# Kernel tuning notes

Hardware: AMD Instinct MI355X
Metric: run time of the kernel (lower is better)

Reference implementation:

```python
import jax, jax.numpy as jnp
import numpy as np

K_POOL = 5

def _conv_lookahead(x, W):
    # Faithful to F.conv2d(pad=(fs//2+1,0)) followed by keeping the last L rows:
    # for fs=3 this reduces to out[t] = sum_j x[t+j] @ W[:,j,:].T (2 trailing zeros).
    # x: [..., L, E], W: [nf, fs, E] -> out [..., L, nf]
    fs = W.shape[1]
    L = x.shape[-2]
    pad = [(0, 0)] * (x.ndim - 2) + [(0, fs - 1), (0, 0)]
    xp = jnp.pad(x, pad)
    out = sum(jnp.einsum('...le,fe->...lf', jax.lax.dynamic_slice_in_dim(xp, j, L, axis=-2), W[:, j, :]) for j in range(fs))
    return out

def _cosine(q, s):
    # q: [B,Q,D], s: [B,S,L,D] -> [B,S,Q,L]
    num = jnp.einsum('bqd,bsld->bsql', q, s)
    qn = jnp.linalg.norm(q, axis=-1)  # [B,Q]
    sn = jnp.linalg.norm(s, axis=-1)  # [B,S,L]
    return num / (qn[:, None, :, None] * sn[:, :, None, :])

def _pool(sim, k=K_POOL):
    # sort-based k-max pooling over last dim -> (max, mean-of-top-k), matching torch.sort + slice
    top = jax.lax.top_k(sim, k)[0]            # [..., Q, k] descending
    return jnp.stack([top[..., 0], top.mean(-1)], axis=-1)  # [..., Q, 2]

def _bce(p, t):
    return -(t * jnp.log(p) + (1.0 - t) * jnp.log(1.0 - p)).mean()

def setup_inputs() -> dict:
    key = jax.random.key(0)
    ks = jax.random.split(key, 9)
    B, S, L, Q, V, E, NF, FS = 16, 48, 64, 32, 50000, 300, 256, 3
    return {
        'sentences': jax.random.randint(ks[0], (B, S, L), 0, V, dtype=jnp.int64 if jax.config.jax_enable_x64 else jnp.int32).astype(jnp.int32),
        'question': jax.random.randint(ks[1], (B, Q), 0, V).astype(jnp.int32),
        'target_sents': jax.random.randint(ks[2], (B, S), 0, 2).astype(jnp.int32),
        'target_docs': jax.random.randint(ks[3], (B,), 0, 2).astype(jnp.int32),
        'similarity_one_hot': jax.random.uniform(ks[4], (B, S, Q, L), dtype=jnp.float32),
        'embeds': jax.random.normal(ks[5], (V, E), dtype=jnp.float32),
        'conv_w': jax.random.normal(ks[6], (NF, FS, E), dtype=jnp.float32),
        'lin_w': jax.random.normal(ks[7], (1, 6), dtype=jnp.float32),
        'lin_b': jax.random.normal(ks[8], (1,), dtype=jnp.float32),
    }

def reference(sentences, question, target_sents, target_docs, similarity_one_hot, embeds, conv_w, lin_w, lin_b):
    q_emb = embeds[question]            # [B,Q,E]
    s_emb = embeds[sentences]           # [B,S,L,E]
    q_conv = _conv_lookahead(q_emb, conv_w)   # [B,Q,NF]
    s_conv = _conv_lookahead(s_emb, conv_w)   # [B,S,L,NF]

    sim_ins = _cosine(q_emb, s_emb)     # [B,S,Q,L]
    qmask = (question > 1).astype(sim_ins.dtype)   # [B,Q]
    smask = (sentences > 1).astype(sim_ins.dtype)  # [B,S,L]
    sim_ins = sim_ins * qmask[:, None, :, None] * smask[:, :, None, :]

    sim_sens = _cosine(q_conv, s_conv)  # [B,S,Q,L]

    feats = jnp.concatenate([_pool(sim_ins), _pool(sim_sens), _pool(similarity_one_hot)], axis=-1)  # [B,S,Q,6]
    lo = jax.nn.sigmoid(jnp.einsum('bsqf,of->bsqo', feats, lin_w)[..., 0] + lin_b[0])  # [B,S,Q]
    sent_output = lo.mean(-1)           # [B,S]

    sal = _bce(sent_output, target_sents.astype(sent_output.dtype))
    doc_emit = sent_output.max(-1)      # [B]
    dal = _bce(doc_emit, target_docs.astype(doc_emit.dtype))
    total_loss = (sal + dal) / 2.0
    return (total_loss, sent_output, doc_emit)
```

## Files before the change

### kernel.cpp

```cpp
#include <hip/hip_runtime.h>
#include <math.h>

#define NB 16
#define NS 48
#define NL 64
#define NQ 32
#define NE 300
#define NF 256
#define KP 320
#define QROWS 36

typedef __attribute__((ext_vector_type(8))) short short8;
typedef __attribute__((ext_vector_type(4))) float f32x4;

#define MFMA(a,b,c) __builtin_amdgcn_mfma_f32_16x16x32_bf16((a),(b),(c),0,0,0)

__device__ __forceinline__ unsigned short f2bf(float f) {
    unsigned u = __float_as_uint(f);
    u += 0x7fff + ((u >> 16) & 1);
    return (unsigned short)(u >> 16);
}

#define SE_PITCH 640
#define SC_PITCH 512
#define SIM_OFF (66 * 640)
#define SIM_PITCH 66
#define DYN_LDS (SIM_OFF + NQ * SIM_PITCH * 4)

__device__ __forceinline__ float wave_reduce_sum(float v) {
#pragma unroll
    for (int off = 32; off; off >>= 1) v += __shfl_xor(v, off, 64);
    return v;
}

__device__ __forceinline__ void top5_pool4(float v0, float v1, float v2, float v3,
                                           int lane, float* mx, float* mn) {
    float s0 = 0.f, s1 = 0.f, s2 = 0.f, s3 = 0.f;
    float x0 = 0.f, x1 = 0.f, x2 = 0.f, x3 = 0.f;
#pragma unroll
    for (int i = 0; i < 5; ++i) {
        float m0 = v0, m1 = v1, m2 = v2, m3 = v3;
#pragma unroll
        for (int off = 32; off; off >>= 1) {
            m0 = fmaxf(m0, __shfl_xor(m0, off, 64));
            m1 = fmaxf(m1, __shfl_xor(m1, off, 64));
            m2 = fmaxf(m2, __shfl_xor(m2, off, 64));
            m3 = fmaxf(m3, __shfl_xor(m3, off, 64));
        }
        if (i == 0) { x0 = m0; x1 = m1; x2 = m2; x3 = m3; }
        s0 += m0; s1 += m1; s2 += m2; s3 += m3;
        unsigned long long k0 = __ballot(v0 == m0);
        unsigned long long k1 = __ballot(v1 == m1);
        unsigned long long k2 = __ballot(v2 == m2);
        unsigned long long k3 = __ballot(v3 == m3);
        if (lane == __ffsll(k0) - 1) v0 = -3.4e38f;
        if (lane == __ffsll(k1) - 1) v1 = -3.4e38f;
        if (lane == __ffsll(k2) - 1) v2 = -3.4e38f;
        if (lane == __ffsll(k3) - 1) v3 = -3.4e38f;
    }
    mx[0] = x0; mx[1] = x1; mx[2] = x2; mx[3] = x3;
    mn[0] = s0 * 0.2f; mn[1] = s1 * 0.2f; mn[2] = s2 * 0.2f; mn[3] = s3 * 0.2f;
}

__global__ __launch_bounds__(256) void prep_kernel(
        const float* __restrict__ conv_w, const int* __restrict__ question,
        const float* __restrict__ embeds,
        short8* __restrict__ Wb2, unsigned short* __restrict__ qe,
        short8* __restrict__ qef, float* __restrict__ q_norm,
        float* __restrict__ qcssq, unsigned int* __restrict__ done_ctr) {
    int blk = blockIdx.x;
    int tid = threadIdx.x;
    if (blk < 120) {
        if (blk == 0 && tid == 0) done_ctr[0] = 0u;
        int i = blk * 256 + tid;
        if (i < NB * NQ) qcssq[i] = 0.f;
        int rl = i & 15;
        int ftile = (i >> 4) & 15;
        int c = i >> 8;
        int kg = c & 3, rest = c >> 2;
        int ks = rest % 10, j = rest / 10;
        int f = ftile * 16 + rl;
        int k0 = ks * 32 + kg * 8;
        const float* src = conv_w + (size_t)(f * 3 + j) * NE;
        short8 h;
#pragma unroll
        for (int e = 0; e < 8; ++e) {
            int k = k0 + e;
            h[e] = (short)((k < NE) ? f2bf(src[k]) : (unsigned short)0);
        }
        Wb2[i] = h;
    } else {
        int row = (blk - 120) * 4 + (tid >> 6);
        int b = row / QROWS, r = row % QROWS;
        int l = tid & 63;
        unsigned short* dst = qe + (size_t)row * KP;
        if (r < NQ) {
            int tok = question[b * NQ + r];
            const float4* rp = (const float4*)(embeds + (size_t)tok * NE);
            short8 h = {0, 0, 0, 0, 0, 0, 0, 0};
            float ss = 0.f;
            if (l < 38) {
                float4 v0 = rp[2 * l];
                ss += v0.x * v0.x + v0.y * v0.y + v0.z * v0.z + v0.w * v0.w;
                h[0] = (short)f2bf(v0.x); h[1] = (short)f2bf(v0.y);
                h[2] = (short)f2bf(v0.z); h[3] = (short)f2bf(v0.w);
                if (2 * l + 1 < 75) {
                    float4 v1 = rp[2 * l + 1];
                    ss += v1.x * v1.x + v1.y * v1.y + v1.z * v1.z + v1.w * v1.w;
                    h[4] = (short)f2bf(v1.x); h[5] = (short)f2bf(v1.y);
                    h[6] = (short)f2bf(v1.z); h[7] = (short)f2bf(v1.w);
                }
            }
            if (l < 40) {
                *(short8*)(dst + 8 * l) = h;
                qef[((size_t)(b * 2 + (r >> 4)) * 40 + l) * 16 + (r & 15)] = h;
            }
            ss = wave_reduce_sum(ss);
            if (l == 0) q_norm[b * NQ + r] = sqrtf(ss);
        } else {
            if (l < 40) {
                short8 z = {0, 0, 0, 0, 0, 0, 0, 0};
                *(short8*)(dst + 8 * l) = z;
            }
        }
    }
}

__global__ __launch_bounds__(256) void qconv_mfma_kernel(
        const unsigned short* __restrict__ qe, const short8* __restrict__ Wb2,
        short8* __restrict__ qcf, float* __restrict__ qcssq) {
    __shared__ unsigned short tile[NQ][72];
    int b = blockIdx.x >> 2, fq = blockIdx.x & 3;
    int tid = threadIdx.x, lane = tid & 63, w = tid >> 6;
    int rl = lane & 15, kg = lane >> 4;
    int ftile = fq * 4 + w;
    f32x4 acc0 = (f32x4){0.f, 0.f, 0.f, 0.f};
    f32x4 acc1 = (f32x4){0.f, 0.f, 0.f, 0.f};
    for (int j = 0; j < 3; ++j) {
#pragma unroll 2
        for (int ks = 0; ks < 10; ++ks) {
            int k = ks * 32 + kg * 8;
            int c = (j * 10 + ks) * 4 + kg;
            short8 a0 = *(const short8*)(qe + ((size_t)(b * QROWS) + rl + j) * KP + k);
            short8 a1 = *(const short8*)(qe + ((size_t)(b * QROWS) + 16 + rl + j) * KP + k);
            short8 bb = Wb2[(c * 16 + ftile) * 16 + rl];
            acc0 = MFMA(a0, bb, acc0);
            acc1 = MFMA(a1, bb, acc1);
        }
    }
    int fl = w * 16 + rl;
#pragma unroll
    for (int reg = 0; reg < 4; ++reg) {
        tile[kg * 4 + reg][fl] = f2bf(acc0[reg]);
        tile[16 + kg * 4 + reg][fl] = f2bf(acc1[reg]);
    }
    __syncthreads();
    {
        int mh = tid >> 7, c_local = (tid >> 4) & 7, rl2 = tid & 15;
        short8 h = *(const short8*)(&tile[mh * 16 + rl2][c_local * 8]);
        qcf[((size_t)(b * 2 + mh) * 32 + 8 * fq + c_local) * 16 + rl2] = h;
    }
    {
        int qq = tid >> 3, fgrp = tid & 7;
        short8 h = *(const short8*)(&tile[qq][fgrp * 8]);
        float ss = 0.f;
#pragma unroll
        for (int e = 0; e < 8; ++e) {
            float v = __uint_as_float(((unsigned)(unsigned short)h[e]) << 16);
            ss += v * v;
        }
        ss += __shfl_xor(ss, 1, 64);
        ss += __shfl_xor(ss, 2, 64);
        ss += __shfl_xor(ss, 4, 64);
        if (fgrp == 0) atomicAdd(&qcssq[b * NQ + qq], ss);
    }
}

extern __shared__ char ldsc[];
__global__ __launch_bounds__(256, 3) void fused8_kernel(
    const int* __restrict__ sentences, const int* __restrict__ question,
    const float* __restrict__ sim_oh, const float* __restrict__ embeds,
    const short8* __restrict__ Wb2,
    const short8* __restrict__ qef, const short8* __restrict__ qcf,
    const float* __restrict__ q_norm, const float* __restrict__ qcssq,
    const float* __restrict__ lin_w, const float* __restrict__ lin_b,
    const int* __restrict__ tsent, const int* __restrict__ tdoc,
    unsigned int* __restrict__ done_ctr,
    float* __restrict__ sent_ws, float* __restrict__ d_out)
{
    __shared__ int toks[NL];
    __shared__ float smaskf[NL], snorm[NL], scnorm[NL];
    __shared__ float qn_s[NQ], qcn_s[NQ], qmf_s[NQ];
    __shared__ float wq[4];
    __shared__ float fpool[NQ][2];
    __shared__ int lastflag;
    __shared__ float red2[4];
    __shared__ float dred[NB];

    int tid = threadIdx.x, lane = tid & 63, w = tid >> 6;
    int rl = lane & 15, kg = lane >> 4;
    int bs = blockIdx.x, b = bs / NS;
    int t = (w << 4) + rl, t7 = t & 7;

    float oh[8];
#pragma unroll
    for (int qi = 0; qi < 8; ++qi) {
        int q = (w << 3) + qi;
        oh[qi] = sim_oh[((size_t)bs * NQ + q) * NL + lane];
    }

    if (tid < NL) {
        int tk = sentences[(size_t)bs * NL + tid];
        toks[tid] = tk;
        smaskf[tid] = (tk > 1) ? 1.f : 0.f;
    } else if (tid < NL + NQ) {
        int q = tid - NL;
        qn_s[q] = q_norm[b * NQ + q];
    } else if (tid < NL + 2 * NQ) {
        int q = tid - NL - NQ;
        qcn_s[q] = sqrtf(qcssq[b * NQ + q]);
    } else if (tid < NL + 3 * NQ) {
        int q = tid - NL - 2 * NQ;
        qmf_s[q] = (question[b * NQ + q] > 1) ? 1.f : 0.f;
    }
    __syncthreads();

#pragma unroll 4
    for (int i = 0; i < 16; ++i) {
        int r = (i << 2) + w;
        char* rowbase = ldsc + r * SE_PITCH;
        int m7 = r & 7;
        const float4* rp = (const float4*)(embeds + (size_t)toks[r] * NE);
        {
            float4 v = rp[lane];
            ushort4 h = {f2bf(v.x), f2bf(v.y), f2bf(v.z), f2bf(v.w)};
            *(ushort4*)(rowbase + (((lane >> 1) ^ m7) << 4) + ((lane & 1) << 3)) = h;
        }
        if (lane < 11) {
            float4 v = rp[64 + lane];
            ushort4 h = {f2bf(v.x), f2bf(v.y), f2bf(v.z), f2bf(v.w)};
            int g = 64 + lane;
            *(ushort4*)(rowbase + (((g >> 1) ^ m7) << 4) + ((g & 1) << 3)) = h;
        }
        if (lane < 5) {
            int pk = 37 + ((lane + 1) >> 1);
            int sub = ((lane + 1) & 1) << 3;
            *(unsigned long long*)(rowbase + ((pk ^ m7) << 4) + sub) = 0ull;
        }
    }
    if (w < 2) {
        int r = 64 + w;
        if (lane < 40) {
            uint4 z = {0, 0, 0, 0};
            *(uint4*)(ldsc + r * SE_PITCH + (lane << 4)) = z;
        }
    }
    __syncthreads();

    {
        f32x4 iacc0 = (f32x4){0.f, 0.f, 0.f, 0.f};
        f32x4 iacc1 = (f32x4){0.f, 0.f, 0.f, 0.f};
        f32x4 nB = (f32x4){0.f, 0.f, 0.f, 0.f};
        const short8* qf = qef + (size_t)(b * 80) * 16;
#pragma unroll 2
        for (int ks = 0; ks < 10; ++ks) {
            int c = ks * 4 + kg;
            short8 bB = *(const short8*)(ldsc + t * SE_PITCH + ((c ^ t7) << 4));
            short8 a0 = qf[c * 16 + rl];
            short8 a1 = qf[(40 + c) * 16 + rl];
            iacc0 = MFMA(a0, bB, iacc0);
            iacc1 = MFMA(a1, bB, iacc1);
            nB = MFMA(bB, bB, nB);
        }
        if (kg == (rl >> 2)) snorm[t] = sqrtf(nB[rl & 3]);
        __syncthreads();

        float inv_t = smaskf[t] / snorm[t];
#pragma unroll
        for (int reg = 0; reg < 4; ++reg) {
            int q0 = kg * 4 + reg;
            float s0 = iacc0[reg] / qn_s[q0] * inv_t * qmf_s[q0];
            *(float*)(ldsc + SIM_OFF + (q0 * SIM_PITCH + t) * 4) = s0;
            int q1 = 16 + kg * 4 + reg;
            float s1 = iacc1[reg] / qn_s[q1] * inv_t * qmf_s[q1];
            *(float*)(ldsc + SIM_OFF + (q1 * SIM_PITCH + t) * 4) = s1;
        }
    }
    __syncthreads();

    {
        int q0 = w << 3;
        float v[8];
#pragma unroll
        for (int qi = 0; qi < 8; ++qi)
            v[qi] = *(float*)(ldsc + SIM_OFF + ((q0 + qi) * SIM_PITCH + lane) * 4);
        float mx[4], mn[4];
        top5_pool4(v[0], v[1], v[2], v[3], lane, mx, mn);
        if (lane == 0)
#pragma unroll
            for (int p = 0; p < 4; ++p) { fpool[q0 + p][0] = mx[p]; fpool[q0 + p][1] = mn[p]; }
        top5_pool4(v[4], v[5], v[6], v[7], lane, mx, mn);
        if (lane == 0)
#pragma unroll
            for (int p = 0; p < 4; ++p) { fpool[q0 + 4 + p][0] = mx[p]; fpool[q0 + 4 + p][1] = mn[p]; }
    }

    f32x4 cacc[4][4];
#pragma unroll
    for (int m = 0; m < 4; ++m)
#pragma unroll
        for (int nn = 0; nn < 4; ++nn) cacc[m][nn] = (f32x4){0.f, 0.f, 0.f, 0.f};
    for (int j = 0; j < 3; ++j) {
#pragma unroll 2
        for (int ks = 0; ks < 10; ++ks) {
            int c = (j * 10 + ks) * 4 + kg;
            short8 a[4], bb[4];
#pragma unroll
            for (int m = 0; m < 4; ++m) {
                int row = m * 16 + rl + j;
                a[m] = *(const short8*)(ldsc + row * SE_PITCH +
                                        ((((ks << 2) + kg) ^ (row & 7)) << 4));
            }
#pragma unroll
            for (int nn = 0; nn < 4; ++nn)
                bb[nn] = Wb2[(c * 16 + (w * 4 + nn)) * 16 + rl];
#pragma unroll
            for (int m = 0; m < 4; ++m)
#pragma unroll
                for (int nn = 0; nn < 4; ++nn)
                    cacc[m][nn] = MFMA(a[m], bb[nn], cacc[m][nn]);
        }
    }
    __syncthreads();

#pragma unroll
    for (int m = 0; m < 4; ++m)
#pragma unroll
        for (int nn = 0; nn < 4; ++nn) {
            int f = (w * 4 + nn) * 16 + rl;
#pragma unroll
            for (int reg = 0; reg < 4; ++reg) {
                int tr = m * 16 + kg * 4 + reg;
                *(unsigned short*)(ldsc + tr * SC_PITCH +
                                   (((f >> 3) ^ (tr & 7)) << 4) + ((f & 7) << 1)) =
                    f2bf(cacc[m][nn][reg]);
            }
        }
    __syncthreads();

    {
        f32x4 sacc0 = (f32x4){0.f, 0.f, 0.f, 0.f};
        f32x4 sacc1 = (f32x4){0.f, 0.f, 0.f, 0.f};
        f32x4 nB = (f32x4){0.f, 0.f, 0.f, 0.f};
        const short8* qc = qcf + (size_t)(b * 64) * 16;
#pragma unroll 2
        for (int ks = 0; ks < 8; ++ks) {
            int c = ks * 4 + kg;
            short8 bB = *(const short8*)(ldsc + t * SC_PITCH + ((c ^ t7) << 4));
            short8 a0 = qc[c * 16 + rl];
            short8 a1 = qc[(32 + c) * 16 + rl];
            sacc0 = MFMA(a0, bB, sacc0);
            sacc1 = MFMA(a1, bB, sacc1);
            nB = MFMA(bB, bB, nB);
        }
        if (kg == (rl >> 2)) scnorm[t] = sqrtf(nB[rl & 3]);
        __syncthreads();

        float inv_t = 1.f / scnorm[t];
#pragma unroll
        for (int reg = 0; reg < 4; ++reg) {
            int q0 = kg * 4 + reg;
            *(float*)(ldsc + SIM_OFF + (q0 * SIM_PITCH + t) * 4) =
                sacc0[reg] / qcn_s[q0] * inv_t;
            int q1 = 16 + kg * 4 + reg;
            *(float*)(ldsc + SIM_OFF + (q1 * SIM_PITCH + t) * 4) =
                sacc1[reg] / qcn_s[q1] * inv_t;
        }
    }
    __syncthreads();

    {
        float lw0 = lin_w[0], lw1 = lin_w[1], lw2 = lin_w[2];
        float lw3 = lin_w[3], lw4 = lin_w[4], lw5 = lin_w[5];
        float lb = lin_b[0];
        int q0 = w << 3;
        float sv[8];
#pragma unroll
        for (int qi = 0; qi < 8; ++qi)
            sv[qi] = *(float*)(ldsc + SIM_OFF + ((q0 + qi) * SIM_PITCH + lane) * 4);
        float mxs[8], mns[8], mxo[8], mno[8];
        top5_pool4(sv[0], sv[1], sv[2], sv[3], lane, mxs, mns);
        top5_pool4(sv[4], sv[5], sv[6], sv[7], lane, mxs + 4, mns + 4);
        top5_pool4(oh[0], oh[1], oh[2], oh[3], lane, mxo, mno);
        top5_pool4(oh[4], oh[5], oh[6], oh[7], lane, mxo + 4, mno + 4);
        float psum = 0.f;
#pragma unroll
        for (int qi = 0; qi < 8; ++qi) {
            float f0 = fpool[q0 + qi][0], f1 = fpool[q0 + qi][1];
            float z = f0 * lw0 + f1 * lw1 + mxs[qi] * lw2 + mns[qi] * lw3 +
                      mxo[qi] * lw4 + mno[qi] * lw5 + lb;
            psum += 1.f / (1.f + expf(-z));
        }
        if (lane == 0) wq[w] = psum;
    }
    __syncthreads();
    if (tid == 0) {
        float sent = (wq[0] + wq[1] + wq[2] + wq[3]) * (1.f / 32.f);
        __hip_atomic_store(&sent_ws[bs], sent, __ATOMIC_RELEASE, __HIP_MEMORY_SCOPE_AGENT);
        d_out[1 + bs] = sent;
        unsigned old = atomicAdd(done_ctr, 1u);
        lastflag = (old == (unsigned)(NB * NS - 1)) ? 1 : 0;
    }
    __syncthreads();

    if (lastflag) {
        float acc_l = 0.f;
        for (int i = tid; i < NB * NS; i += 256) {
            float p = __hip_atomic_load(&sent_ws[i], __ATOMIC_ACQUIRE, __HIP_MEMORY_SCOPE_AGENT);
            float tt2 = (float)tsent[i];
            acc_l += tt2 * logf(p) + (1.f - tt2) * logf(1.f - p);
        }
        acc_l = wave_reduce_sum(acc_l);
        if ((tid & 63) == 0) red2[tid >> 6] = acc_l;
        if (tid < NB) {
            float m = -3.4e38f;
            for (int s = 0; s < NS; ++s)
                m = fmaxf(m, __hip_atomic_load(&sent_ws[tid * NS + s], __ATOMIC_ACQUIRE,
                                               __HIP_MEMORY_SCOPE_AGENT));
            d_out[1 + NB * NS + tid] = m;
            float tt2 = (float)tdoc[tid];
            dred[tid] = tt2 * logf(m) + (1.f - tt2) * logf(1.f - m);
        }
        __syncthreads();
        if (tid == 0) {
            float sal = -(red2[0] + red2[1] + red2[2] + red2[3]) / (float)(NB * NS);
            float dsum = 0.f;
            for (int i = 0; i < NB; ++i) dsum += dred[i];
            float dal = -dsum / (float)NB;
            d_out[0] = 0.5f * (sal + dal);
        }
    }
}

extern "C" void kernel_launch(void* const* d_in, const int* in_sizes, int n_in,
                              void* d_out, int out_size, void* d_ws, size_t ws_size,
                              hipStream_t stream) {
    const int* sentences = (const int*)d_in[0];
    const int* question = (const int*)d_in[1];
    const int* tsent = (const int*)d_in[2];
    const int* tdoc = (const int*)d_in[3];
    const float* sim_oh = (const float*)d_in[4];
    const float* embeds = (const float*)d_in[5];
    const float* conv_w = (const float*)d_in[6];
    const float* lin_w = (const float*)d_in[7];
    const float* lin_b = (const float*)d_in[8];
    float* out = (float*)d_out;

    char* wsc = (char*)d_ws;
    short8* Wb2            = (short8*)(wsc);
    unsigned short* qe_old = (unsigned short*)(wsc + 491520);
    short8* qef            = (short8*)(wsc + 860160);
    short8* qcf            = (short8*)(wsc + 1187840);
    float* q_norm          = (float*)(wsc + 1449984);
    float* qcssq           = (float*)(wsc + 1452032);
    float* sent_ws         = (float*)(wsc + 1454080);
    unsigned int* done_ctr = (unsigned int*)(wsc + 1457152);

    hipFuncSetAttribute(reinterpret_cast<const void*>(fused8_kernel),
                        hipFuncAttributeMaxDynamicSharedMemorySize, DYN_LDS);

    prep_kernel<<<264, 256, 0, stream>>>(conv_w, question, embeds,
                                         Wb2, qe_old, qef, q_norm, qcssq, done_ctr);
    qconv_mfma_kernel<<<NB * 4, 256, 0, stream>>>(qe_old, Wb2, qcf, qcssq);
    fused8_kernel<<<NB * NS, 256, DYN_LDS, stream>>>(
        sentences, question, sim_oh, embeds, Wb2, qef, qcf, q_norm, qcssq,
        lin_w, lin_b, tsent, tdoc, done_ctr, sent_ws, out);
}
```

Measured before the change: 126.2 us.

## Replace wave-wide top-5 pooling with per-lane sorted top-5 plus 8-lane merge

Top-k pooling is reworked so each lane holds 8 contiguous elements of one query row and keeps a sorted top-5 list in registers. Five 3-step shuffle reductions within 8-lane groups then replace the previous 6-step full-wave reductions done for four rows at a time. The one-hot similarity loads become float4 vector loads, and the LDS round-trip through the pooled-feature buffer is removed. The aim is fewer shuffles and ballots in the pooling phases, at the cost of more registers for the sorting network.

Measured after the change: 113.2 us. 1.12x faster.

```diff
diff --git a/kernel.cpp b/kernel.cpp
--- a/kernel.cpp
+++ b/kernel.cpp
@@ -33,33 +33,36 @@
     return v;
 }
 
-__device__ __forceinline__ void top5_pool4(float v0, float v1, float v2, float v3,
-                                           int lane, float* mx, float* mn) {
-    float s0 = 0.f, s1 = 0.f, s2 = 0.f, s3 = 0.f;
-    float x0 = 0.f, x1 = 0.f, x2 = 0.f, x3 = 0.f;
+__device__ __forceinline__ void top5_pool_g8(const float* v, int lane,
+                                             float& mx, float& mn) {
+    const float NEG = -3.4e38f;
+    float s0 = NEG, s1 = NEG, s2 = NEG, s3 = NEG, s4 = NEG;
+#pragma unroll
+    for (int e = 0; e < 8; ++e) {
+        float x = v[e], t;
+        t = fmaxf(s0, x); x = fminf(s0, x); s0 = t;
+        t = fmaxf(s1, x); x = fminf(s1, x); s1 = t;
+        t = fmaxf(s2, x); x = fminf(s2, x); s2 = t;
+        t = fmaxf(s3, x); x = fminf(s3, x); s3 = t;
+        t = fmaxf(s4, x); x = fminf(s4, x); s4 = t;
+    }
+    int gb = lane & 56;
+    int j = lane & 7;
+    float sum = 0.f, first = 0.f;
 #pragma unroll
     for (int i = 0; i < 5; ++i) {
-        float m0 = v0, m1 = v1, m2 = v2, m3 = v3;
-#pragma unroll
-        for (int off = 32; off; off >>= 1) {
-            m0 = fmaxf(m0, __shfl_xor(m0, off, 64));
-            m1 = fmaxf(m1, __shfl_xor(m1, off, 64));
-            m2 = fmaxf(m2, __shfl_xor(m2, off, 64));
-            m3 = fmaxf(m3, __shfl_xor(m3, off, 64));
-        }
-        if (i == 0) { x0 = m0; x1 = m1; x2 = m2; x3 = m3; }
-        s0 += m0; s1 += m1; s2 += m2; s3 += m3;
-        unsigned long long k0 = __ballot(v0 == m0);
-        unsigned long long k1 = __ballot(v1 == m1);
-        unsigned long long k2 = __ballot(v2 == m2);
-        unsigned long long k3 = __ballot(v3 == m3);
-        if (lane == __ffsll(k0) - 1) v0 = -3.4e38f;
-        if (lane == __ffsll(k1) - 1) v1 = -3.4e38f;
-        if (lane == __ffsll(k2) - 1) v2 = -3.4e38f;
-        if (lane == __ffsll(k3) - 1) v3 = -3.4e38f;
-    }
-    mx[0] = x0; mx[1] = x1; mx[2] = x2; mx[3] = x3;
-    mn[0] = s0 * 0.2f; mn[1] = s1 * 0.2f; mn[2] = s2 * 0.2f; mn[3] = s3 * 0.2f;
+        float m = s0;
+        m = fmaxf(m, __shfl_xor(m, 1, 64));
+        m = fmaxf(m, __shfl_xor(m, 2, 64));
+        m = fmaxf(m, __shfl_xor(m, 4, 64));
+        if (i == 0) first = m;
+        sum += m;
+        unsigned long long bal = __ballot(s0 == m);
+        int leader = __ffsll((unsigned long long)((bal >> gb) & 0xffull)) - 1;
+        if (j == leader) { s0 = s1; s1 = s2; s2 = s3; s3 = s4; s4 = NEG; }
+    }
+    mx = first;
+    mn = sum * 0.2f;
 }
 
 __global__ __launch_bounds__(256) void prep_kernel(
@@ -177,7 +180,7 @@
 }
 
 extern __shared__ char ldsc[];
-__global__ __launch_bounds__(256, 3) void fused8_kernel(
+__global__ __launch_bounds__(256, 3) void fused9_kernel(
     const int* __restrict__ sentences, const int* __restrict__ question,
     const float* __restrict__ sim_oh, const float* __restrict__ embeds,
     const short8* __restrict__ Wb2,
@@ -192,7 +195,6 @@
     __shared__ float smaskf[NL], snorm[NL], scnorm[NL];
     __shared__ float qn_s[NQ], qcn_s[NQ], qmf_s[NQ];
     __shared__ float wq[4];
-    __shared__ float fpool[NQ][2];
     __shared__ int lastflag;
     __shared__ float red2[4];
     __shared__ float dred[NB];
@@ -201,12 +203,15 @@
     int rl = lane & 15, kg = lane >> 4;
     int bs = blockIdx.x, b = bs / NS;
     int t = (w << 4) + rl, t7 = t & 7;
-
-    float oh[8];
-#pragma unroll
-    for (int qi = 0; qi < 8; ++qi) {
-        int q = (w << 3) + qi;
-        oh[qi] = sim_oh[((size_t)bs * NQ + q) * NL + lane];
+    int pg = lane >> 3, pj = lane & 7;
+
+    float ohv[8];
+    {
+        const float* ohp = sim_oh + ((size_t)bs * NQ + (w << 3) + pg) * NL + (pj << 3);
+        float4 o0 = *(const float4*)(ohp);
+        float4 o1 = *(const float4*)(ohp + 4);
+        ohv[0] = o0.x; ohv[1] = o0.y; ohv[2] = o0.z; ohv[3] = o0.w;
+        ohv[4] = o1.x; ohv[5] = o1.y; ohv[6] = o1.z; ohv[7] = o1.w;
     }
 
     if (tid < NL) {
@@ -288,21 +293,17 @@
     }
     __syncthreads();
 
-    {
-        int q0 = w << 3;
+    float f_i0, f_i1;
+    {
+        const float* basep = (const float*)(ldsc + SIM_OFF) +
+                             ((w << 3) + pg) * SIM_PITCH + (pj << 3);
         float v[8];
 #pragma unroll
-        for (int qi = 0; qi < 8; ++qi)
-            v[qi] = *(float*)(ldsc + SIM_OFF + ((q0 + qi) * SIM_PITCH + lane) * 4);
-        float mx[4], mn[4];
-        top5_pool4(v[0], v[1], v[2], v[3], lane, mx, mn);
-        if (lane == 0)
-#pragma unroll
-            for (int p = 0; p < 4; ++p) { fpool[q0 + p][0] = mx[p]; fpool[q0 + p][1] = mn[p]; }
-        top5_pool4(v[4], v[5], v[6], v[7], lane, mx, mn);
-        if (lane == 0)
-#pragma unroll
-            for (int p = 0; p < 4; ++p) { fpool[q0 + 4 + p][0] = mx[p]; fpool[q0 + 4 + p][1] = mn[p]; }
+        for (int e = 0; e < 8; e += 2) {
+            float2 p = *(const float2*)(basep + e);
+            v[e] = p.x; v[e + 1] = p.y;
+        }
+        top5_pool_g8(v, lane, f_i0, f_i1);
     }
 
     f32x4 cacc[4][4];
@@ -383,25 +384,23 @@
         float lw0 = lin_w[0], lw1 = lin_w[1], lw2 = lin_w[2];
         float lw3 = lin_w[3], lw4 = lin_w[4], lw5 = lin_w[5];
         float lb = lin_b[0];
-        int q0 = w << 3;
+        const float* basep = (const float*)(ldsc + SIM_OFF) +
+                             ((w << 3) + pg) * SIM_PITCH + (pj << 3);
         float sv[8];
 #pragma unroll
-        for (int qi = 0; qi < 8; ++qi)
-            sv[qi] = *(float*)(ldsc + SIM_OFF + ((q0 + qi) * SIM_PITCH + lane) * 4);
-        float mxs[8], mns[8], mxo[8], mno[8];
-        top5_pool4(sv[0], sv[1], sv[2], sv[3], lane, mxs, mns);
-        top5_pool4(sv[4], sv[5], sv[6], sv[7], lane, mxs + 4, mns + 4);
-        top5_pool4(oh[0], oh[1], oh[2], oh[3], lane, mxo, mno);
-        top5_pool4(oh[4], oh[5], oh[6], oh[7], lane, mxo + 4, mno + 4);
-        float psum = 0.f;
-#pragma unroll
-        for (int qi = 0; qi < 8; ++qi) {
-            float f0 = fpool[q0 + qi][0], f1 = fpool[q0 + qi][1];
-            float z = f0 * lw0 + f1 * lw1 + mxs[qi] * lw2 + mns[qi] * lw3 +
-                      mxo[qi] * lw4 + mno[qi] * lw5 + lb;
-            psum += 1.f / (1.f + expf(-z));
-        }
-        if (lane == 0) wq[w] = psum;
+        for (int e = 0; e < 8; e += 2) {
+            float2 p = *(const float2*)(basep + e);
+            sv[e] = p.x; sv[e + 1] = p.y;
+        }
+        float mxs, mns, mxo, mno;
+        top5_pool_g8(sv, lane, mxs, mns);
+        top5_pool_g8(ohv, lane, mxo, mno);
+        float z = f_i0 * lw0 + f_i1 * lw1 + mxs * lw2 + mns * lw3 +
+                  mxo * lw4 + mno * lw5 + lb;
+        float p = 1.f / (1.f + expf(-z));
+        float contrib = (pj == 0) ? p : 0.f;
+        contrib = wave_reduce_sum(contrib);
+        if (lane == 0) wq[w] = contrib;
     }
     __syncthreads();
     if (tid == 0) {
@@ -466,13 +465,13 @@
     float* sent_ws         = (float*)(wsc + 1454080);
     unsigned int* done_ctr = (unsigned int*)(wsc + 1457152);
 
-    hipFuncSetAttribute(reinterpret_cast<const void*>(fused8_kernel),
+    hipFuncSetAttribute(reinterpret_cast<const void*>(fused9_kernel),
                         hipFuncAttributeMaxDynamicSharedMemorySize, DYN_LDS);
 
     prep_kernel<<<264, 256, 0, stream>>>(conv_w, question, embeds,
                                          Wb2, qe_old, qef, q_norm, qcssq, done_ctr);
     qconv_mfma_kernel<<<NB * 4, 256, 0, stream>>>(qe_old, Wb2, qcf, qcssq);
-    fused8_kernel<<<NB * NS, 256, DYN_LDS, stream>>>(
+    fused9_kernel<<<NB * NS, 256, DYN_LDS, stream>>>(
         sentences, question, sim_oh, embeds, Wb2, qef, qcf, q_norm, qcssq,
         lin_w, lin_b, tsent, tdoc, done_ctr, sent_ws, out);
 }
```
